# Kernel tuning notes

Hardware: AMD Instinct MI355X
Metric: run time of the kernel (lower is better)

The kernel has to match this reference:

```python
import jax, jax.numpy as jnp
import numpy as np

N_NODES = 100000
N_EDGES = 1600000
D_FEAT = 64
K = 5


def setup_inputs() -> dict:
    key = jax.random.key(0)
    k1, k2, k3 = jax.random.split(key, 3)
    feat = jax.random.normal(k1, (N_NODES, D_FEAT), dtype=jnp.float32)
    theta = jnp.asarray([1.0, -0.8, 0.45, -0.2, 0.08], dtype=jnp.float32)
    src = jax.random.randint(k2, (N_EDGES,), 0, N_NODES, dtype=jnp.int32)
    dst = jax.random.randint(k3, (N_EDGES,), 0, N_NODES, dtype=jnp.int32)
    return {"feat": feat, "theta": theta, "src": src, "dst": dst}


def reference(feat, theta, src, dst):
    n = feat.shape[0]
    # in-degrees: number of edges terminating at each node, clamped to >= 1
    deg = jax.ops.segment_sum(jnp.ones_like(dst, dtype=feat.dtype), dst, num_segments=n)
    d_invsqrt = jnp.maximum(deg, 1.0) ** -0.5  # [N]
    d_invsqrt = d_invsqrt[:, None]  # [N, 1]

    def unn_laplacian(x):
        scaled = x * d_invsqrt  # [N, D]
        agg = jax.ops.segment_sum(scaled[src], dst, num_segments=n)  # [N, D]
        return x - agg * d_invsqrt

    h = theta[0] * feat
    for k in range(1, theta.shape[0]):
        feat = unn_laplacian(feat)
        h = h + theta[k] * feat
    return h
```

## Files before the change

kernel.cpp:

```cpp
#include <hip/hip_runtime.h>
#include <hip/hip_bf16.h>
#include <hip/hip_fp16.h>

#define WG 256
#define WGB 1024
#define D 64
#define MAXNB 1024

typedef unsigned long long u64;
typedef unsigned int u32x4 __attribute__((ext_vector_type(4)));
typedef float f32x4 __attribute__((ext_vector_type(4)));

__device__ inline float ld_mixed(const void* p, int bf, long i) {
    if (bf) {
        unsigned short u = ((const unsigned short*)p)[i];
        return __uint_as_float(((unsigned int)u) << 16);
    }
    return ((const float*)p)[i];
}


__global__ __launch_bounds__(WGB) void kc_hist(
        const int* __restrict__ dst, int E, int NBc, int CPB,
        int* __restrict__ histmat,
        const void* __restrict__ theta, int* __restrict__ flag) {
    __shared__ int h[MAXNB];
    int B = blockIdx.x, t = threadIdx.x;
    if (B == 0 && t == 0) {
        unsigned int w = *(const unsigned int*)theta;
        *flag = (w == 0x3F800000u) ? 0 : 1;
    }
    for (int i = t; i < NBc; i += WGB) h[i] = 0;
    __syncthreads();
    int base = B * CPB;
    int end = min(base + CPB, E);
    for (int e = base + t; e < end; e += WGB)
        atomicAdd(&h[dst[e] >> 8], 1);
    __syncthreads();
    for (int i = t; i < NBc; i += WGB)
        histmat[(long)i * NBc + B] = h[i];
}

__global__ void k_scan1(const int* __restrict__ in, int M,
                        int* __restrict__ out, int* __restrict__ part) {
    __shared__ int s[WG];
    int g = blockIdx.x * WG + threadIdx.x;
    int t = threadIdx.x;
    int v0 = (g < M) ? in[g] : 0;
    s[t] = v0;
    __syncthreads();
    for (int o = 1; o < WG; o <<= 1) {
        int v = (t >= o) ? s[t - o] : 0;
        __syncthreads();
        s[t] += v;
        __syncthreads();
    }
    if (g < M) out[g] = s[t] - v0;
    if (t == WG - 1) part[blockIdx.x] = s[t];
}

__global__ __launch_bounds__(WGB) void kc_scatter(
        const int* __restrict__ src, const int* __restrict__ dst, int E,
        int NBc, int CPB, const int* __restrict__ outx,
        const int* __restrict__ part, int P,
        unsigned int* __restrict__ tmp) {
    __shared__ int off[MAXNB];
    __shared__ int ps[1024];
    __shared__ int pex[1024];
    int B = blockIdx.x, t = threadIdx.x;
    int pv = (t < P) ? part[t] : 0;
    ps[t] = pv;
    __syncthreads();
    for (int o = 1; o < 1024; o <<= 1) {
        int v = (t >= o) ? ps[t - o] : 0;
        __syncthreads();
        ps[t] += v;
        __syncthreads();
    }
    pex[t] = ps[t] - pv;
    __syncthreads();
    for (int i = t; i < NBc; i += WGB) {
        long g = (long)i * NBc + B;
        off[i] = outx[g] + pex[g >> 8];
    }
    __syncthreads();
    int base = B * CPB;
    int end = min(base + CPB, E);
    for (int e = base + t; e < end; e += WGB) {
        int d = dst[e];
        int pos = atomicAdd(&off[d >> 8], 1);
        tmp[pos] = (unsigned)src[e] | ((unsigned)(d & 255) << 24);
    }
}

__global__ __launch_bounds__(WGB) void kf(
        const unsigned int* __restrict__ tmp, const int* __restrict__ outx,
        const int* __restrict__ part, int P,
        int NBc, int N, int E, int* __restrict__ ptr,
        float* __restrict__ dinv, float* __restrict__ dsqrt,
        int* __restrict__ csr) {
    __shared__ int h[256];
    __shared__ int pfx[256];
    __shared__ int cnt[256];
    __shared__ int ps[1024];
    __shared__ int pex[1024];
    int B = blockIdx.x, t = threadIdx.x;
    int pv = (t < P) ? part[t] : 0;
    ps[t] = pv;
    __syncthreads();
    for (int o = 1; o < 1024; o <<= 1) {
        int v = (t >= o) ? ps[t - o] : 0;
        __syncthreads();
        ps[t] += v;
        __syncthreads();
    }
    pex[t] = ps[t] - pv;
    __syncthreads();
    long g1 = (long)B * NBc;
    int rbase = outx[g1] + pex[g1 >> 8];
    int rend;
    if (B == NBc - 1) rend = E;
    else {
        long g2 = (long)(B + 1) * NBc;
        rend = outx[g2] + pex[g2 >> 8];
    }
    if (t < 256) h[t] = 0;
    __syncthreads();
    for (int e = rbase + t; e < rend; e += WGB)
        atomicAdd(&h[tmp[e] >> 24], 1);
    __syncthreads();
    if (t < 256) pfx[t] = h[t];
    __syncthreads();
    for (int o = 1; o < 256; o <<= 1) {
        int v = 0;
        if (t < 256 && t >= o) v = pfx[t - o];
        __syncthreads();
        if (t < 256) pfx[t] += v;
        __syncthreads();
    }
    if (t < 256) {
        int ex = pfx[t] - h[t];
        int node = B * 256 + t;
        if (node < N) {
            ptr[node] = rbase + ex;
            float d = (float)h[t];
            d = d < 1.f ? 1.f : d;
            dinv[node]  = rsqrtf(d);
            dsqrt[node] = sqrtf(d);
        }
        cnt[t] = rbase + ex;
    }
    if (B == 0 && t == 0) ptr[N] = E;
    __syncthreads();
    for (int e = rbase + t; e < rend; e += WGB) {
        unsigned p = tmp[e];
        int pos = atomicAdd(&cnt[p >> 24], 1);
        csr[pos] = (int)(p & 0xFFFFFF);
    }
}


__global__ void k_init(const void* __restrict__ feat, const void* __restrict__ theta,
                       const int* __restrict__ flag, const float* __restrict__ dinv,
                       long NF, __half* __restrict__ xs, __half* __restrict__ h) {
    int bf = *flag;
    long g = ((long)blockIdx.x * WG + threadIdx.x) * 8;
    if (g < NF) {
        float th0 = ld_mixed(theta, bf, 0);
        float w = dinv[g >> 6];
        float f[8];
#pragma unroll
        for (int j = 0; j < 8; ++j) f[j] = ld_mixed(feat, bf, g + j);
        __half2 a0 = __floats2half2_rn(f[0] * w, f[1] * w);
        __half2 a1 = __floats2half2_rn(f[2] * w, f[3] * w);
        __half2 a2 = __floats2half2_rn(f[4] * w, f[5] * w);
        __half2 a3 = __floats2half2_rn(f[6] * w, f[7] * w);
        __half2 b0 = __floats2half2_rn(th0 * f[0], th0 * f[1]);
        __half2 b1 = __floats2half2_rn(th0 * f[2], th0 * f[3]);
        __half2 b2 = __floats2half2_rn(th0 * f[4], th0 * f[5]);
        __half2 b3 = __floats2half2_rn(th0 * f[6], th0 * f[7]);
        u32x4 xo, ho;
        xo.x = *(const unsigned*)&a0; xo.y = *(const unsigned*)&a1;
        xo.z = *(const unsigned*)&a2; xo.w = *(const unsigned*)&a3;
        ho.x = *(const unsigned*)&b0; ho.y = *(const unsigned*)&b1;
        ho.z = *(const unsigned*)&b2; ho.w = *(const unsigned*)&b3;
        __builtin_nontemporal_store(xo, (u32x4*)xs + (g >> 3));
        __builtin_nontemporal_store(ho, (u32x4*)h  + (g >> 3));
    }
}

__global__ __launch_bounds__(WG) void k_spmv(
        const __half* __restrict__ xs,
        const float* __restrict__ dinv, const float* __restrict__ dsqrt,
        const int* __restrict__ ptr, const int* __restrict__ csr,
        const void* __restrict__ theta, const int* __restrict__ flag, int k,
        int N, __half* __restrict__ xsn, __half* __restrict__ h,
        void* __restrict__ out, int last) {
    int wv   = (int)(((unsigned)blockIdx.x * blockDim.x + threadIdx.x) >> 6);
    int lane = threadIdx.x & 63;
    int node = 4 * wv + (lane >> 4);
    int l    = lane & 15;
    bool valid = node < N;
    int nc = valid ? node : 0;
    int s0 = ptr[nc];
    int s1 = valid ? ptr[nc + 1] : s0;

    const uint2* xs4 = (const uint2*)xs;
    float ax = 0.f, ay = 0.f, az = 0.f, aw = 0.f;
    int e = s0;
    for (; e + 8 <= s1; e += 8) {
        int idx[8];
#pragma unroll
        for (int j = 0; j < 8; ++j) idx[j] = csr[e + j];
        uint2 a[8];
#pragma unroll
        for (int j = 0; j < 8; ++j) a[j] = xs4[idx[j] * 16 + l];
#pragma unroll
        for (int j = 0; j < 8; ++j) {
            float2 f0 = __half22float2(*(const __half2*)&a[j].x);
            float2 f1 = __half22float2(*(const __half2*)&a[j].y);
            ax += f0.x; ay += f0.y; az += f1.x; aw += f1.y;
        }
    }
    if (e + 4 <= s1) {
        int idx[4];
#pragma unroll
        for (int j = 0; j < 4; ++j) idx[j] = csr[e + j];
        uint2 a[4];
#pragma unroll
        for (int j = 0; j < 4; ++j) a[j] = xs4[idx[j] * 16 + l];
#pragma unroll
        for (int j = 0; j < 4; ++j) {
            float2 f0 = __half22float2(*(const __half2*)&a[j].x);
            float2 f1 = __half22float2(*(const __half2*)&a[j].y);
            ax += f0.x; ay += f0.y; az += f1.x; aw += f1.y;
        }
        e += 4;
    }
    for (; e < s1; ++e) {
        uint2 av = xs4[csr[e] * 16 + l];
        float2 f0 = __half22float2(*(const __half2*)&av.x);
        float2 f1 = __half22float2(*(const __half2*)&av.y);
        ax += f0.x; ay += f0.y; az += f1.x; aw += f1.y;
    }

    if (!valid) return;
    int o = node * 16 + l;
    float w  = dinv[node];
    float ds = dsqrt[node];
    uint2 xv = xs4[o];
    float2 x0 = __half22float2(*(const __half2*)&xv.x);
    float2 x1 = __half22float2(*(const __half2*)&xv.y);
    float v0 = x0.x * ds - w * ax;
    float v1 = x0.y * ds - w * ay;
    float v2 = x1.x * ds - w * az;
    float v3 = x1.y * ds - w * aw;
    int bf = *flag;
    float th = ld_mixed(theta, bf, k);
    u64 hb = __builtin_nontemporal_load((const u64*)h + o);
    unsigned hlo = (unsigned)hb, hhi = (unsigned)(hb >> 32);
    float2 h0 = __half22float2(*(const __half2*)&hlo);
    float2 h1 = __half22float2(*(const __half2*)&hhi);
    h0.x += th * v0; h0.y += th * v1;
    h1.x += th * v2; h1.y += th * v3;
    if (last) {
        if (bf) {
            __hip_bfloat162 b0, b1;
            b0.x = __float2bfloat16(h0.x); b0.y = __float2bfloat16(h0.y);
            b1.x = __float2bfloat16(h1.x); b1.y = __float2bfloat16(h1.y);
            u64 r = (u64)(*(const unsigned*)&b0) |
                    ((u64)(*(const unsigned*)&b1) << 32);
            __builtin_nontemporal_store(r, (u64*)out + o);
        } else {
            f32x4 r; r.x = h0.x; r.y = h0.y; r.z = h1.x; r.w = h1.y;
            __builtin_nontemporal_store(r, (f32x4*)out + o);
        }
    } else {
        __half2 t0 = __floats2half2_rn(v0 * w, v1 * w);
        __half2 t1 = __floats2half2_rn(v2 * w, v3 * w);
        __half2 u0 = __floats2half2_rn(h0.x, h0.y);
        __half2 u1 = __floats2half2_rn(h1.x, h1.y);
        u64 xo64 = (u64)(*(const unsigned*)&t0) |
                   ((u64)(*(const unsigned*)&t1) << 32);
        u64 ho64 = (u64)(*(const unsigned*)&u0) |
                   ((u64)(*(const unsigned*)&u1) << 32);
        __builtin_nontemporal_store(xo64, (u64*)xsn + o);
        __builtin_nontemporal_store(ho64, (u64*)h   + o);
    }
}

extern "C" void kernel_launch(void* const* d_in, const int* in_sizes, int n_in,
                              void* d_out, int out_size, void* d_ws, size_t ws_size,
                              hipStream_t stream) {
    const void* feat  = d_in[0];
    const void* theta = d_in[1];
    const int*  src   = (const int*)d_in[2];
    const int*  dst   = (const int*)d_in[3];
    long NF = in_sizes[0];
    int  N  = (int)(NF / D);
    int  E  = in_sizes[2];

    int NBc = (N + 255) >> 8;
    int CPB = (E + NBc - 1) / NBc;
    int M   = NBc * NBc;
    int sbl = (M + WG - 1) / WG;

    char* w = (char*)d_ws;
    size_t off = 0;
    auto alloc = [&](size_t b) -> void* {
        void* p = w + off;
        off = (off + b + 255) & ~(size_t)255;
        return p;
    };
    int*      histmat = (int*)alloc((size_t)M * 4);
    int*      outx    = (int*)alloc((size_t)M * 4);
    int*      part    = (int*)alloc(1024 * 4);
    unsigned* tmp     = (unsigned*)alloc((size_t)E * 4);
    int*      ptr     = (int*)alloc(((size_t)N + 1) * 4);
    int*      csr     = (int*)alloc((size_t)E * 4);
    float*    dinv    = (float*)alloc((size_t)N * 4);
    float*    dsqrt   = (float*)alloc((size_t)N * 4);
    int*      flag    = (int*)alloc(4);
    __half*   xs_a    = (__half*)alloc((size_t)NF * 2);
    __half*   xs_b    = (__half*)alloc((size_t)NF * 2);
    __half*   h       = (__half*)alloc((size_t)NF * 2);

    int fbl = (int)((NF / 8 + WG - 1) / WG);
    int wbl = (((N + 3) / 4) + 3) / 4;

    kc_hist<<<NBc, WGB, 0, stream>>>(dst, E, NBc, CPB, histmat, theta, flag);
    k_scan1<<<sbl, WG, 0, stream>>>(histmat, M, outx, part);
    kc_scatter<<<NBc, WGB, 0, stream>>>(src, dst, E, NBc, CPB, outx, part, sbl, tmp);
    kf<<<NBc, WGB, 0, stream>>>(tmp, outx, part, sbl, NBc, N, E, ptr, dinv, dsqrt, csr);
    k_init<<<fbl, WG, 0, stream>>>(feat, theta, flag, dinv, NF, xs_a, h);

    __half* xa = xs_a;
    __half* xb = xs_b;
    for (int k = 1; k <= 4; ++k) {
        int last = (k == 4);
        k_spmv<<<wbl, WG, 0, stream>>>(xa, dinv, dsqrt, ptr, csr, theta, flag, k,
                                       N, xb, h, d_out, last);
        __half* t = xa; xa = xb; xb = t;
    }
}
```

Measured before the change: 283.4 us.

## Stage CSR indices in LDS and defer the h accumulation by one step

Each 256-thread block now covers 16 nodes and first copies those nodes' CSR neighbor indices into shared memory, then gathers from LDS, falling back to global reads when a block has more than 2048 edges. The h update is shifted one iteration later: it uses the previous x, recovered as xs*dsqrt, so the first SpMV skips reading and writing h entirely and the last step adds both remaining terms. Nontemporal loads and stores are replaced with ordinary ones. The shared-memory staging adds a block barrier and some LDS traffic in exchange for fewer global index reads and one less h round trip.

Result: faster. 261.4 us (-7.8%).

```diff
diff --git a/kernel.cpp b/kernel.cpp
--- a/kernel.cpp
+++ b/kernel.cpp
@@ -6,6 +6,7 @@
 #define WGB 1024
 #define D 64
 #define MAXNB 1024
+#define CSRCAP 2048
 
 typedef unsigned long long u64;
 typedef unsigned int u32x4 __attribute__((ext_vector_type(4)));
@@ -184,10 +185,50 @@
         xo.z = *(const unsigned*)&a2; xo.w = *(const unsigned*)&a3;
         ho.x = *(const unsigned*)&b0; ho.y = *(const unsigned*)&b1;
         ho.z = *(const unsigned*)&b2; ho.w = *(const unsigned*)&b3;
-        __builtin_nontemporal_store(xo, (u32x4*)xs + (g >> 3));
-        __builtin_nontemporal_store(ho, (u32x4*)h  + (g >> 3));
-    }
-}
+        ((u32x4*)xs)[g >> 3] = xo;
+        ((u32x4*)h)[g >> 3]  = ho;
+    }
+}
+
+#define SPMV_LOOPS(FETCH)                                                  \
+    for (; e + 8 <= s1; e += 8) {                                          \
+        int idx[8];                                                        \
+        _Pragma("unroll")                                                  \
+        for (int j = 0; j < 8; ++j) idx[j] = FETCH(e + j);                 \
+        uint2 a[8];                                                        \
+        _Pragma("unroll")                                                  \
+        for (int j = 0; j < 8; ++j) a[j] = xs4[idx[j] * 16 + l];           \
+        _Pragma("unroll")                                                  \
+        for (int j = 0; j < 8; ++j) {                                      \
+            float2 f0 = __half22float2(*(const __half2*)&a[j].x);          \
+            float2 f1 = __half22float2(*(const __half2*)&a[j].y);          \
+            ax += f0.x; ay += f0.y; az += f1.x; aw += f1.y;                \
+        }                                                                  \
+    }                                                                      \
+    if (e + 4 <= s1) {                                                     \
+        int idx[4];                                                        \
+        _Pragma("unroll")                                                  \
+        for (int j = 0; j < 4; ++j) idx[j] = FETCH(e + j);                 \
+        uint2 a[4];                                                        \
+        _Pragma("unroll")                                                  \
+        for (int j = 0; j < 4; ++j) a[j] = xs4[idx[j] * 16 + l];           \
+        _Pragma("unroll")                                                  \
+        for (int j = 0; j < 4; ++j) {                                      \
+            float2 f0 = __half22float2(*(const __half2*)&a[j].x);          \
+            float2 f1 = __half22float2(*(const __half2*)&a[j].y);          \
+            ax += f0.x; ay += f0.y; az += f1.x; aw += f1.y;                \
+        }                                                                  \
+        e += 4;                                                            \
+    }                                                                      \
+    for (; e < s1; ++e) {                                                  \
+        uint2 av = xs4[FETCH(e) * 16 + l];                                 \
+        float2 f0 = __half22float2(*(const __half2*)&av.x);                \
+        float2 f1 = __half22float2(*(const __half2*)&av.y);                \
+        ax += f0.x; ay += f0.y; az += f1.x; aw += f1.y;                    \
+    }
+
+#define FETCH_L(x) lcs[(x) - rb]
+#define FETCH_G(x) csr[x]
 
 __global__ __launch_bounds__(WG) void k_spmv(
         const __half* __restrict__ xs,
@@ -196,10 +237,23 @@
         const void* __restrict__ theta, const int* __restrict__ flag, int k,
         int N, __half* __restrict__ xsn, __half* __restrict__ h,
         void* __restrict__ out, int last) {
-    int wv   = (int)(((unsigned)blockIdx.x * blockDim.x + threadIdx.x) >> 6);
-    int lane = threadIdx.x & 63;
-    int node = 4 * wv + (lane >> 4);
+    __shared__ int lcs[CSRCAP];
+    int t = threadIdx.x;
+    int nodeBase = blockIdx.x * 16;
+    int lane = t & 63;
+    int node = nodeBase + 4 * (t >> 6) + (lane >> 4);
     int l    = lane & 15;
+
+    int nbEnd = min(nodeBase + 16, N);
+    int rb = ptr[nodeBase];
+    int re = ptr[nbEnd];
+    int cntb = re - rb;
+    bool useL = (cntb <= CSRCAP);
+    if (useL) {
+        for (int i = t; i < cntb; i += WG) lcs[i] = csr[rb + i];
+    }
+    __syncthreads();
+
     bool valid = node < N;
     int nc = valid ? node : 0;
     int s0 = ptr[nc];
@@ -208,40 +262,10 @@
     const uint2* xs4 = (const uint2*)xs;
     float ax = 0.f, ay = 0.f, az = 0.f, aw = 0.f;
     int e = s0;
-    for (; e + 8 <= s1; e += 8) {
-        int idx[8];
-#pragma unroll
-        for (int j = 0; j < 8; ++j) idx[j] = csr[e + j];
-        uint2 a[8];
-#pragma unroll
-        for (int j = 0; j < 8; ++j) a[j] = xs4[idx[j] * 16 + l];
-#pragma unroll
-        for (int j = 0; j < 8; ++j) {
-            float2 f0 = __half22float2(*(const __half2*)&a[j].x);
-            float2 f1 = __half22float2(*(const __half2*)&a[j].y);
-            ax += f0.x; ay += f0.y; az += f1.x; aw += f1.y;
-        }
-    }
-    if (e + 4 <= s1) {
-        int idx[4];
-#pragma unroll
-        for (int j = 0; j < 4; ++j) idx[j] = csr[e + j];
-        uint2 a[4];
-#pragma unroll
-        for (int j = 0; j < 4; ++j) a[j] = xs4[idx[j] * 16 + l];
-#pragma unroll
-        for (int j = 0; j < 4; ++j) {
-            float2 f0 = __half22float2(*(const __half2*)&a[j].x);
-            float2 f1 = __half22float2(*(const __half2*)&a[j].y);
-            ax += f0.x; ay += f0.y; az += f1.x; aw += f1.y;
-        }
-        e += 4;
-    }
-    for (; e < s1; ++e) {
-        uint2 av = xs4[csr[e] * 16 + l];
-        float2 f0 = __half22float2(*(const __half2*)&av.x);
-        float2 f1 = __half22float2(*(const __half2*)&av.y);
-        ax += f0.x; ay += f0.y; az += f1.x; aw += f1.y;
+    if (useL) {
+        SPMV_LOOPS(FETCH_L)
+    } else {
+        SPMV_LOOPS(FETCH_G)
     }
 
     if (!valid) return;
@@ -251,19 +275,30 @@
     uint2 xv = xs4[o];
     float2 x0 = __half22float2(*(const __half2*)&xv.x);
     float2 x1 = __half22float2(*(const __half2*)&xv.y);
-    float v0 = x0.x * ds - w * ax;
-    float v1 = x0.y * ds - w * ay;
-    float v2 = x1.x * ds - w * az;
-    float v3 = x1.y * ds - w * aw;
+    float u0 = x0.x * ds, u1 = x0.y * ds, u2 = x1.x * ds, u3 = x1.y * ds;
+    float v0 = u0 - w * ax;
+    float v1 = u1 - w * ay;
+    float v2 = u2 - w * az;
+    float v3 = u3 - w * aw;
     int bf = *flag;
-    float th = ld_mixed(theta, bf, k);
-    u64 hb = __builtin_nontemporal_load((const u64*)h + o);
-    unsigned hlo = (unsigned)hb, hhi = (unsigned)(hb >> 32);
-    float2 h0 = __half22float2(*(const __half2*)&hlo);
-    float2 h1 = __half22float2(*(const __half2*)&hhi);
-    h0.x += th * v0; h0.y += th * v1;
-    h1.x += th * v2; h1.y += th * v3;
+    if (k == 1) {
+        __half2 t0 = __floats2half2_rn(v0 * w, v1 * w);
+        __half2 t1 = __floats2half2_rn(v2 * w, v3 * w);
+        uint2 xo;
+        xo.x = *(const unsigned*)&t0; xo.y = *(const unsigned*)&t1;
+        ((uint2*)xsn)[o] = xo;
+        return;
+    }
+    float thp = ld_mixed(theta, bf, k - 1);
+    uint2 hv = ((const uint2*)h)[o];
+    float2 h0 = __half22float2(*(const __half2*)&hv.x);
+    float2 h1 = __half22float2(*(const __half2*)&hv.y);
+    h0.x += thp * u0; h0.y += thp * u1;
+    h1.x += thp * u2; h1.y += thp * u3;
     if (last) {
+        float thl = ld_mixed(theta, bf, k);
+        h0.x += thl * v0; h0.y += thl * v1;
+        h1.x += thl * v2; h1.y += thl * v3;
         if (bf) {
             __hip_bfloat162 b0, b1;
             b0.x = __float2bfloat16(h0.x); b0.y = __float2bfloat16(h0.y);
@@ -278,14 +313,13 @@
     } else {
         __half2 t0 = __floats2half2_rn(v0 * w, v1 * w);
         __half2 t1 = __floats2half2_rn(v2 * w, v3 * w);
-        __half2 u0 = __floats2half2_rn(h0.x, h0.y);
-        __half2 u1 = __floats2half2_rn(h1.x, h1.y);
-        u64 xo64 = (u64)(*(const unsigned*)&t0) |
-                   ((u64)(*(const unsigned*)&t1) << 32);
-        u64 ho64 = (u64)(*(const unsigned*)&u0) |
-                   ((u64)(*(const unsigned*)&u1) << 32);
-        __builtin_nontemporal_store(xo64, (u64*)xsn + o);
-        __builtin_nontemporal_store(ho64, (u64*)h   + o);
+        __half2 u0h = __floats2half2_rn(h0.x, h0.y);
+        __half2 u1h = __floats2half2_rn(h1.x, h1.y);
+        uint2 xo, ho;
+        xo.x = *(const unsigned*)&t0;  xo.y = *(const unsigned*)&t1;
+        ho.x = *(const unsigned*)&u0h; ho.y = *(const unsigned*)&u1h;
+        ((uint2*)xsn)[o] = xo;
+        ((uint2*)h)[o]   = ho;
     }
 }
 
@@ -326,7 +360,7 @@
     __half*   h       = (__half*)alloc((size_t)NF * 2);
 
     int fbl = (int)((NF / 8 + WG - 1) / WG);
-    int wbl = (((N + 3) / 4) + 3) / 4;
+    int wbl = (N + 15) / 16;
 
     kc_hist<<<NBc, WGB, 0, stream>>>(dst, E, NBc, CPB, histmat, theta, flag);
     k_scan1<<<sbl, WG, 0, stream>>>(histmat, M, outx, part);
```
